# Performance work log

Measured on AMD Instinct MI355X. Metric: run time of the kernel, lower is better.

The kernel has to match this reference:

```python
import jax, jax.numpy as jnp
import numpy as np

N = 100000   # num nodes
E = 1200000  # num edges (avg degree ~12)
D = 64       # emb_dim


def setup_inputs() -> dict:
    key = jax.random.key(0)
    k1, k2, k3, k4, k5, k6 = jax.random.split(key, 6)
    x = jax.random.normal(k1, (N, D), dtype=jnp.float32)
    edge_index = jax.random.randint(k2, (2, E), 0, N, dtype=jnp.int64)
    edge_attr = jax.random.normal(k3, (E, D), dtype=jnp.float32)
    W = jax.random.normal(k4, (D, D), dtype=jnp.float32) * 0.05  # Linear weight
    b = jax.random.normal(k5, (D,), dtype=jnp.float32) * 0.05    # Linear bias
    root_emb = jax.random.normal(k6, (D,), dtype=jnp.float32)
    return {"x": x, "edge_index": edge_index, "edge_attr": edge_attr,
            "W": W, "b": b, "root_emb": root_emb}


def reference(x, edge_index, edge_attr, W, b, root_emb):
    n = x.shape[0]
    x = x @ W.T + b  # Linear(emb_dim, emb_dim)
    row, col = edge_index[0], edge_index[1]
    ones_e = jnp.ones(row.shape[0], dtype=x.dtype)
    # degrees initialized to ones then index_add of ones per edge endpoint
    deg_i = 1.0 + jax.ops.segment_sum(ones_e, row, num_segments=n)
    deg_j = 1.0 + jax.ops.segment_sum(ones_e, col, num_segments=n)
    dinv_i = deg_i ** -0.5
    dinv_j = deg_j ** -0.5
    val = dinv_i[row] * dinv_j[col]  # [E] normalized edge weights
    # spmm(adj_t, x) + message_edge both scatter val-weighted terms to `row`;
    # fuse into a single gather->scale->segment_sum pass (identical math).
    agg = jax.ops.segment_sum(val[:, None] * (x[col] + edge_attr), row,
                              num_segments=n)  # [N, D]
    node_feat = jax.nn.relu(agg) + jax.nn.relu(x + root_emb) * (dinv_i * dinv_j)[:, None]
    return node_feat
```

## Files before the change

kernel.cpp:

```cpp
#include <hip/hip_runtime.h>

#define N_NODES 100000
#define N_EDGES 1200000
#define DIM     64
#define SCAN_B  256
#define NB      ((N_NODES + SCAN_B - 1) / SCAN_B)
#define LIN_BLOCKS (N_NODES / 16)
#define CNT_BLOCKS ((N_EDGES / 4 + 255) / 256)

typedef unsigned short ushort_t;

__device__ inline float bf2f(ushort_t u) {
    return __uint_as_float(((unsigned int)u) << 16);
}
__device__ inline ushort_t f2bf(float f) {
    unsigned int x = __float_as_uint(f);
    unsigned int r = x + 0x7fff + ((x >> 16) & 1);
    return (ushort_t)(r >> 16);
}

__global__ __launch_bounds__(256) void prep_kernel(
        const float* __restrict__ x, const float* __restrict__ W,
        const float* __restrict__ b, ushort_t* __restrict__ xwb,
        const int* __restrict__ row, const int* __restrict__ col,
        int* __restrict__ cnt_r, int* __restrict__ cnt_c,
        int* __restrict__ rank) {
    __shared__ float sWt[DIM * (DIM + 1)];
    __shared__ float sx[16][DIM];

    int t = threadIdx.x;

    if (blockIdx.x >= LIN_BLOCKS) {
        int i = (blockIdx.x - LIN_BLOCKS) * 256 + t;
        if (i * 4 >= N_EDGES) return;
        int4 r4 = ((const int4*)row)[i];
        int4 c4 = ((const int4*)col)[i];
        int4 rk;
        rk.x = atomicAdd(&cnt_r[r4.x], 1);
        rk.y = atomicAdd(&cnt_r[r4.y], 1);
        rk.z = atomicAdd(&cnt_r[r4.z], 1);
        rk.w = atomicAdd(&cnt_r[r4.w], 1);
        ((int4*)rank)[i] = rk;
        atomicAdd(&cnt_c[c4.x], 1);
        atomicAdd(&cnt_c[c4.y], 1);
        atomicAdd(&cnt_c[c4.z], 1);
        atomicAdd(&cnt_c[c4.w], 1);
        return;
    }

    int row0 = blockIdx.x * 16;
    for (int i = t; i < DIM * DIM; i += 256) {
        int d = i >> 6, k = i & 63;
        sWt[k * (DIM + 1) + d] = W[i];
    }
    {
        int lr = t >> 4, off = (t & 15) << 2;
        const float4 v = *(const float4*)(x + (size_t)(row0 + lr) * DIM + off);
        sx[lr][off + 0] = v.x; sx[lr][off + 1] = v.y;
        sx[lr][off + 2] = v.z; sx[lr][off + 3] = v.w;
    }
    __syncthreads();

    int d  = t & 63;
    int r0 = (t >> 6) * 4;

    float bd = b[d];
    float a0 = bd, a1 = bd, a2 = bd, a3 = bd;
    const float2* x0 = (const float2*)sx[r0 + 0];
    const float2* x1 = (const float2*)sx[r0 + 1];
    const float2* x2 = (const float2*)sx[r0 + 2];
    const float2* x3 = (const float2*)sx[r0 + 3];
    #pragma unroll
    for (int k2 = 0; k2 < DIM / 2; k2++) {
        float w0 = sWt[(2 * k2 + 0) * (DIM + 1) + d];
        float w1 = sWt[(2 * k2 + 1) * (DIM + 1) + d];
        float2 v0 = x0[k2], v1 = x1[k2], v2 = x2[k2], v3 = x3[k2];
        a0 = fmaf(v0.x, w0, a0); a0 = fmaf(v0.y, w1, a0);
        a1 = fmaf(v1.x, w0, a1); a1 = fmaf(v1.y, w1, a1);
        a2 = fmaf(v2.x, w0, a2); a2 = fmaf(v2.y, w1, a2);
        a3 = fmaf(v3.x, w0, a3); a3 = fmaf(v3.y, w1, a3);
    }
    size_t base = (size_t)(row0 + r0) * DIM + d;
    xwb[base + 0 * DIM] = f2bf(a0);
    xwb[base + 1 * DIM] = f2bf(a1);
    xwb[base + 2 * DIM] = f2bf(a2);
    xwb[base + 3 * DIM] = f2bf(a3);
}

__global__ void scan_a(const int* __restrict__ cnt_r, const int* __restrict__ cnt_c,
                       int* __restrict__ offsets, int* __restrict__ partials,
                       float* __restrict__ dinv_i, float* __restrict__ dinv_j) {
    __shared__ int s[SCAN_B];
    int t = threadIdx.x;
    int i = blockIdx.x * SCAN_B + t;
    int v = (i < N_NODES) ? cnt_r[i] : 0;
    if (i < N_NODES) {
        dinv_i[i] = rsqrtf(1.0f + (float)v);
        dinv_j[i] = rsqrtf(1.0f + (float)cnt_c[i]);
    }
    s[t] = v;
    __syncthreads();
    for (int off = 1; off < SCAN_B; off <<= 1) {
        int add = (t >= off) ? s[t - off] : 0;
        __syncthreads();
        s[t] += add;
        __syncthreads();
    }
    if (i < N_NODES) offsets[i] = s[t] - v;
    if (t == SCAN_B - 1) partials[blockIdx.x] = s[t];
}

__global__ void scan_c(int* __restrict__ offsets, const int* __restrict__ partials) {
    __shared__ int sred[SCAN_B];
    int t = threadIdx.x, bid = blockIdx.x;
    int v = 0;
    for (int j = t; j < NB; j += SCAN_B)
        if (j < bid) v += partials[j];
    sred[t] = v;
    __syncthreads();
    for (int off = SCAN_B / 2; off > 0; off >>= 1) {
        if (t < off) sred[t] += sred[t + off];
        __syncthreads();
    }
    int base = sred[0];
    int i = bid * SCAN_B + t;
    if (i < N_NODES) offsets[i] += base;
}

__global__ void bin_kernel(const int* __restrict__ row, const int* __restrict__ col,
                           const int* __restrict__ rank, const int* __restrict__ offsets,
                           int2* __restrict__ rec) {
    int i = blockIdx.x * blockDim.x + threadIdx.x;
    if (i * 4 >= N_EDGES) return;
    int4 r4 = ((const int4*)row)[i];
    int4 c4 = ((const int4*)col)[i];
    int4 k4 = ((const int4*)rank)[i];
    int e = i * 4;
    rec[offsets[r4.x] + k4.x] = make_int2(e + 0, c4.x);
    rec[offsets[r4.y] + k4.y] = make_int2(e + 1, c4.y);
    rec[offsets[r4.z] + k4.z] = make_int2(e + 2, c4.z);
    rec[offsets[r4.w] + k4.w] = make_int2(e + 3, c4.w);
}

__global__ __launch_bounds__(256) void gather_kernel(
        const int* __restrict__ offsets, const int* __restrict__ cnt_r,
        const int2* __restrict__ rec,
        const float* __restrict__ edge_attr, const ushort_t* __restrict__ xwb,
        const float* __restrict__ dinv_i, const float* __restrict__ dinv_j,
        const float* __restrict__ root, float* __restrict__ out) {
    int lane = threadIdx.x & 63;
    int g    = lane >> 4;
    int q    = (lane & 15) << 2;
    int n    = blockIdx.x * 4 + (threadIdx.x >> 6);

    int   start = offsets[n];
    int   cnt   = cnt_r[n];
    float di    = dinv_i[n];

    const ushort4 xun0 = *(const ushort4*)(xwb + (size_t)n * DIM + q);
    const float4  rt   = *(const float4*)(root + q);
    const float   vj0  = dinv_j[n];

    float4 acc = make_float4(0.f, 0.f, 0.f, 0.f);
    int k = g;
    if (k < cnt) {
        int2 rcB = rec[start + k];
        int2 rcC = rec[start + k + 4];
        float4  ea = *(const float4*)(edge_attr + (size_t)rcB.x * DIM + q);
        ushort4 xu = *(const ushort4*)(xwb + (size_t)rcB.y * DIM + q);
        float   vj = dinv_j[rcB.y];
        for (;;) {
            int  kn   = k + 4;
            bool more = kn < cnt;
            int2 rcD  = rec[start + k + 8];
            float4 ean; ushort4 xun; float vjn;
            if (more) {
                ean = *(const float4*)(edge_attr + (size_t)rcC.x * DIM + q);
                xun = *(const ushort4*)(xwb + (size_t)rcC.y * DIM + q);
                vjn = dinv_j[rcC.y];
            }
            float vv = di * vj;
            acc.x = fmaf(vv, ea.x + bf2f(xu.x), acc.x);
            acc.y = fmaf(vv, ea.y + bf2f(xu.y), acc.y);
            acc.z = fmaf(vv, ea.z + bf2f(xu.z), acc.z);
            acc.w = fmaf(vv, ea.w + bf2f(xu.w), acc.w);
            if (!more) break;
            k = kn; ea = ean; xu = xun; vj = vjn; rcC = rcD;
        }
    }

    acc.x += __shfl_xor(acc.x, 16); acc.y += __shfl_xor(acc.y, 16);
    acc.z += __shfl_xor(acc.z, 16); acc.w += __shfl_xor(acc.w, 16);
    acc.x += __shfl_xor(acc.x, 32); acc.y += __shfl_xor(acc.y, 32);
    acc.z += __shfl_xor(acc.z, 32); acc.w += __shfl_xor(acc.w, 32);

    if (g == 0) {
        float s = di * vj0;
        float4 o;
        o.x = fmaxf(acc.x, 0.f) + fmaxf(bf2f(xun0.x) + rt.x, 0.f) * s;
        o.y = fmaxf(acc.y, 0.f) + fmaxf(bf2f(xun0.y) + rt.y, 0.f) * s;
        o.z = fmaxf(acc.z, 0.f) + fmaxf(bf2f(xun0.z) + rt.z, 0.f) * s;
        o.w = fmaxf(acc.w, 0.f) + fmaxf(bf2f(xun0.w) + rt.w, 0.f) * s;
        *(float4*)(out + (size_t)n * DIM + q) = o;
    }
}

extern "C" void kernel_launch(void* const* d_in, const int* in_sizes, int n_in,
                              void* d_out, int out_size, void* d_ws, size_t ws_size,
                              hipStream_t stream) {
    const float* x         = (const float*)d_in[0];
    const int*   edge_idx  = (const int*)d_in[1];
    const float* edge_attr = (const float*)d_in[2];
    const float* W         = (const float*)d_in[3];
    const float* b         = (const float*)d_in[4];
    const float* root_emb  = (const float*)d_in[5];
    float*       out       = (float*)d_out;

    const int* row = edge_idx;
    const int* col = edge_idx + N_EDGES;

    char* ws = (char*)d_ws;
    ushort_t* xwb      = (ushort_t*)ws;   ws += (size_t)N_NODES * DIM * 2;
    int*      cnt_r    = (int*)ws;        ws += (size_t)N_NODES * 4;
    int*      cnt_c    = (int*)ws;        ws += (size_t)N_NODES * 4;
    float*    dinv_i   = (float*)ws;      ws += (size_t)N_NODES * 4;
    float*    dinv_j   = (float*)ws;      ws += (size_t)N_NODES * 4;
    int*      offsets  = (int*)ws;        ws += (size_t)N_NODES * 4;
    int*      partials = (int*)ws;        ws += 1024 * 4;
    int*      rank     = (int*)ws;        ws += (size_t)N_EDGES * 4;
    int2*     rec      = (int2*)ws;       ws += (size_t)N_EDGES * 8;

    hipMemsetAsync(cnt_r, 0, (size_t)N_NODES * 2 * sizeof(int), stream);

    prep_kernel<<<LIN_BLOCKS + CNT_BLOCKS, 256, 0, stream>>>(
        x, W, b, xwb, row, col, cnt_r, cnt_c, rank);

    scan_a<<<NB, SCAN_B, 0, stream>>>(cnt_r, cnt_c, offsets, partials, dinv_i, dinv_j);
    scan_c<<<NB, SCAN_B, 0, stream>>>(offsets, partials);

    bin_kernel<<<CNT_BLOCKS, 256, 0, stream>>>(row, col, rank, offsets, rec);

    gather_kernel<<<N_NODES / 4, 256, 0, stream>>>(
        offsets, cnt_r, rec, edge_attr, xwb, dinv_i, dinv_j, root_emb, out);
}
```

Baseline: 604.5 us.

## Deepen gather prefetch pipeline, widen linear tile, use nontemporal loads and stores

The gather loop now keeps two edges' worth of edge_attr, xwb and dinv_j loads in flight instead of one, to hide more random-access latency. edge_attr and x are read, and the output written, with nontemporal hints so streaming data does not evict the reused xwb rows from cache. The linear-projection part of prep_kernel processes 32 rows per block with 8 accumulators per thread and float4 shared-memory reads, which reuses each W load more. The cost is higher register pressure in both kernels, which may lower occupancy.

```diff
diff --git a/kernel.cpp b/kernel.cpp
--- a/kernel.cpp
+++ b/kernel.cpp
@@ -5,10 +5,12 @@
 #define DIM     64
 #define SCAN_B  256
 #define NB      ((N_NODES + SCAN_B - 1) / SCAN_B)
-#define LIN_BLOCKS (N_NODES / 16)
+#define LIN_ROWS   32
+#define LIN_BLOCKS (N_NODES / LIN_ROWS)
 #define CNT_BLOCKS ((N_EDGES / 4 + 255) / 256)
 
 typedef unsigned short ushort_t;
+typedef float f4 __attribute__((ext_vector_type(4)));
 
 __device__ inline float bf2f(ushort_t u) {
     return __uint_as_float(((unsigned int)u) << 16);
@@ -26,7 +28,7 @@
         int* __restrict__ cnt_r, int* __restrict__ cnt_c,
         int* __restrict__ rank) {
     __shared__ float sWt[DIM * (DIM + 1)];
-    __shared__ float sx[16][DIM];
+    __shared__ f4    sx4[LIN_ROWS][DIM / 4];
 
     int t = threadIdx.x;
 
@@ -48,43 +50,41 @@
         return;
     }
 
-    int row0 = blockIdx.x * 16;
+    int row0 = blockIdx.x * LIN_ROWS;
     for (int i = t; i < DIM * DIM; i += 256) {
         int d = i >> 6, k = i & 63;
         sWt[k * (DIM + 1) + d] = W[i];
     }
-    {
-        int lr = t >> 4, off = (t & 15) << 2;
-        const float4 v = *(const float4*)(x + (size_t)(row0 + lr) * DIM + off);
-        sx[lr][off + 0] = v.x; sx[lr][off + 1] = v.y;
-        sx[lr][off + 2] = v.z; sx[lr][off + 3] = v.w;
+    for (int i = t; i < LIN_ROWS * (DIM / 4); i += 256) {
+        int r = i >> 4, kq = i & 15;
+        sx4[r][kq] = __builtin_nontemporal_load(
+            (const f4*)(x + (size_t)(row0 + r) * DIM + (kq << 2)));
     }
     __syncthreads();
 
     int d  = t & 63;
-    int r0 = (t >> 6) * 4;
+    int rg = (t >> 6) * 8;
 
     float bd = b[d];
-    float a0 = bd, a1 = bd, a2 = bd, a3 = bd;
-    const float2* x0 = (const float2*)sx[r0 + 0];
-    const float2* x1 = (const float2*)sx[r0 + 1];
-    const float2* x2 = (const float2*)sx[r0 + 2];
-    const float2* x3 = (const float2*)sx[r0 + 3];
+    float a[8];
     #pragma unroll
-    for (int k2 = 0; k2 < DIM / 2; k2++) {
-        float w0 = sWt[(2 * k2 + 0) * (DIM + 1) + d];
-        float w1 = sWt[(2 * k2 + 1) * (DIM + 1) + d];
-        float2 v0 = x0[k2], v1 = x1[k2], v2 = x2[k2], v3 = x3[k2];
-        a0 = fmaf(v0.x, w0, a0); a0 = fmaf(v0.y, w1, a0);
-        a1 = fmaf(v1.x, w0, a1); a1 = fmaf(v1.y, w1, a1);
-        a2 = fmaf(v2.x, w0, a2); a2 = fmaf(v2.y, w1, a2);
-        a3 = fmaf(v3.x, w0, a3); a3 = fmaf(v3.y, w1, a3);
-    }
-    size_t base = (size_t)(row0 + r0) * DIM + d;
-    xwb[base + 0 * DIM] = f2bf(a0);
-    xwb[base + 1 * DIM] = f2bf(a1);
-    xwb[base + 2 * DIM] = f2bf(a2);
-    xwb[base + 3 * DIM] = f2bf(a3);
+    for (int r = 0; r < 8; r++) a[r] = bd;
+
+    #pragma unroll
+    for (int kq = 0; kq < DIM / 4; kq++) {
+        float w0 = sWt[(4 * kq + 0) * (DIM + 1) + d];
+        float w1 = sWt[(4 * kq + 1) * (DIM + 1) + d];
+        float w2 = sWt[(4 * kq + 2) * (DIM + 1) + d];
+        float w3 = sWt[(4 * kq + 3) * (DIM + 1) + d];
+        #pragma unroll
+        for (int r = 0; r < 8; r++) {
+            f4 v = sx4[rg + r][kq];
+            a[r] = fmaf(v.w, w3, fmaf(v.z, w2, fmaf(v.y, w1, fmaf(v.x, w0, a[r]))));
+        }
+    }
+    #pragma unroll
+    for (int r = 0; r < 8; r++)
+        xwb[(size_t)(row0 + rg + r) * DIM + d] = f2bf(a[r]);
 }
 
 __global__ void scan_a(const int* __restrict__ cnt_r, const int* __restrict__ cnt_c,
@@ -158,34 +158,47 @@
     float di    = dinv_i[n];
 
     const ushort4 xun0 = *(const ushort4*)(xwb + (size_t)n * DIM + q);
-    const float4  rt   = *(const float4*)(root + q);
+    const f4      rt   = *(const f4*)(root + q);
     const float   vj0  = dinv_j[n];
 
-    float4 acc = make_float4(0.f, 0.f, 0.f, 0.f);
+    f4 acc = {0.f, 0.f, 0.f, 0.f};
     int k = g;
     if (k < cnt) {
-        int2 rcB = rec[start + k];
-        int2 rcC = rec[start + k + 4];
-        float4  ea = *(const float4*)(edge_attr + (size_t)rcB.x * DIM + q);
-        ushort4 xu = *(const ushort4*)(xwb + (size_t)rcB.y * DIM + q);
-        float   vj = dinv_j[rcB.y];
+        int2 rc0 = rec[start + k];
+        int2 rc1 = rec[start + k + 4];
+        int2 rc2 = rec[start + k + 8];
+        f4 ea0 = __builtin_nontemporal_load(
+            (const f4*)(edge_attr + (size_t)rc0.x * DIM + q));
+        ushort4 xu0 = *(const ushort4*)(xwb + (size_t)rc0.y * DIM + q);
+        float   vjA = dinv_j[rc0.y];
+        bool m1 = (k + 4) < cnt;
+        f4 ea1; ushort4 xu1; float vjB;
+        if (m1) {
+            ea1 = __builtin_nontemporal_load(
+                (const f4*)(edge_attr + (size_t)rc1.x * DIM + q));
+            xu1 = *(const ushort4*)(xwb + (size_t)rc1.y * DIM + q);
+            vjB = dinv_j[rc1.y];
+        }
         for (;;) {
-            int  kn   = k + 4;
-            bool more = kn < cnt;
-            int2 rcD  = rec[start + k + 8];
-            float4 ean; ushort4 xun; float vjn;
-            if (more) {
-                ean = *(const float4*)(edge_attr + (size_t)rcC.x * DIM + q);
-                xun = *(const ushort4*)(xwb + (size_t)rcC.y * DIM + q);
-                vjn = dinv_j[rcC.y];
+            bool m2 = (k + 8) < cnt;
+            int2 rc3 = rec[start + k + 12];
+            f4 ea2; ushort4 xu2; float vjC;
+            if (m2) {
+                ea2 = __builtin_nontemporal_load(
+                    (const f4*)(edge_attr + (size_t)rc2.x * DIM + q));
+                xu2 = *(const ushort4*)(xwb + (size_t)rc2.y * DIM + q);
+                vjC = dinv_j[rc2.y];
             }
-            float vv = di * vj;
-            acc.x = fmaf(vv, ea.x + bf2f(xu.x), acc.x);
-            acc.y = fmaf(vv, ea.y + bf2f(xu.y), acc.y);
-            acc.z = fmaf(vv, ea.z + bf2f(xu.z), acc.z);
-            acc.w = fmaf(vv, ea.w + bf2f(xu.w), acc.w);
-            if (!more) break;
-            k = kn; ea = ean; xu = xun; vj = vjn; rcC = rcD;
+            float vv = di * vjA;
+            acc.x = fmaf(vv, ea0.x + bf2f(xu0.x), acc.x);
+            acc.y = fmaf(vv, ea0.y + bf2f(xu0.y), acc.y);
+            acc.z = fmaf(vv, ea0.z + bf2f(xu0.z), acc.z);
+            acc.w = fmaf(vv, ea0.w + bf2f(xu0.w), acc.w);
+            if (!m1) break;
+            k += 4;
+            ea0 = ea1; xu0 = xu1; vjA = vjB;
+            ea1 = ea2; xu1 = xu2; vjB = vjC;
+            m1 = m2; rc2 = rc3;
         }
     }
 
@@ -196,12 +209,12 @@
 
     if (g == 0) {
         float s = di * vj0;
-        float4 o;
+        f4 o;
         o.x = fmaxf(acc.x, 0.f) + fmaxf(bf2f(xun0.x) + rt.x, 0.f) * s;
         o.y = fmaxf(acc.y, 0.f) + fmaxf(bf2f(xun0.y) + rt.y, 0.f) * s;
         o.z = fmaxf(acc.z, 0.f) + fmaxf(bf2f(xun0.z) + rt.z, 0.f) * s;
         o.w = fmaxf(acc.w, 0.f) + fmaxf(bf2f(xun0.w) + rt.w, 0.f) * s;
-        *(float4*)(out + (size_t)n * DIM + q) = o;
+        __builtin_nontemporal_store(o, (f4*)(out + (size_t)n * DIM + q));
     }
 }
 
```

After: 601.1 us. No clear change (-0.6%).
